# Kernel tuning notes

Measured on AMD Instinct MI355X. Metric: run time of the kernel, lower is better.

## Reference

```python
import jax, jax.numpy as jnp
import numpy as np

B, H, W, C = 16, 64, 64, 768
NH, KD = 12, 64           # num_heads, key_dim; C == NH*KD
NUM_AXES = 2              # attn_axes = [[1],[2]] -> heads split into 2 groups
SCALE = float(np.sqrt(KD))


def setup_inputs() -> dict:
    key = jax.random.key(0)
    ks = jax.random.split(key, 8)
    s = 0.02  # init scale for kernels
    return {
        "queries": jax.random.normal(ks[0], (B, H, W, C), dtype=jnp.float32),
        "values": jax.random.normal(ks[1], (B, H, W, C), dtype=jnp.float32),
        "Wq": jax.random.normal(ks[2], (C, NH, KD), dtype=jnp.float32) * s,
        "bq": jnp.zeros((NH, KD), dtype=jnp.float32),
        "Wk": jax.random.normal(ks[3], (C, NH, KD), dtype=jnp.float32) * s,
        "bk": jnp.zeros((NH, KD), dtype=jnp.float32),
        "Wv": jax.random.normal(ks[4], (C, NH, KD), dtype=jnp.float32) * s,
        "bv": jnp.zeros((NH, KD), dtype=jnp.float32),
        "Wo": jax.random.normal(ks[5], (NH, KD, C), dtype=jnp.float32) * s,
        "bo": jnp.zeros((C,), dtype=jnp.float32),
    }


def _attend_axis_h(q, k, v):
    # attention along the H axis (axis 1); q,k,v: [B,H,W,n,d]
    s = jnp.einsum('bxwnd,bhwnd->bwnhx', k, q) / SCALE  # [B,W,n,Hq,Hk]
    s = jax.nn.softmax(s, axis=-1)
    return jnp.einsum('bwnhx,bxwnd->bhwnd', s, v)


def _attend_axis_w(q, k, v):
    # attention along the W axis (axis 2); q,k,v: [B,H,W,n,d]
    s = jnp.einsum('bhynd,bhwnd->bhnwy', k, q) / SCALE  # [B,H,n,Wq,Wk]
    s = jax.nn.softmax(s, axis=-1)
    return jnp.einsum('bhnwy,bhynd->bhwnd', s, v)


def reference(queries, values, Wq, bq, Wk, bk, Wv, bv, Wo, bo):
    # QKV projections: [B,H,W,C] -> [B,H,W,NH,KD]
    q = jnp.einsum('bhwc,cnd->bhwnd', queries, Wq) + bq
    k = jnp.einsum('bhwc,cnd->bhwnd', values, Wk) + bk
    v = jnp.einsum('bhwc,cnd->bhwnd', values, Wv) + bv
    g = NH // NUM_AXES  # heads per axis group
    o0 = _attend_axis_h(q[..., :g, :], k[..., :g, :], v[..., :g, :])
    o1 = _attend_axis_w(q[..., g:, :], k[..., g:, :], v[..., g:, :])
    out = jnp.concatenate([o0, o1], axis=-2)  # [B,H,W,NH,KD]
    return jnp.einsum('bhwnd,ndc->bhwc', out, Wo) + bo
```

## Files before the change

kernel.cpp:

```cpp
#include <hip/hip_runtime.h>

typedef unsigned short u16;
typedef __bf16 bf16x8 __attribute__((ext_vector_type(8)));
typedef float f32x4 __attribute__((ext_vector_type(4)));

union BF8 {
    bf16x8 v;
    __bf16 e[8];
    u16 h[8];
};

typedef __attribute__((address_space(1))) void gvoid;
typedef __attribute__((address_space(3))) void lvoid;

__device__ __forceinline__ u16 f2bf(float f) {
    __bf16 h = (__bf16)f;
    return __builtin_bit_cast(u16, h);
}

__device__ __forceinline__ void gld_lds16(const void* g, void* l) {
    __builtin_amdgcn_global_load_lds((gvoid*)g, (lvoid*)l, 16, 0, 0);
}

__device__ __forceinline__ f32x4 mfma16(bf16x8 a, bf16x8 b, f32x4 c) {
    return __builtin_amdgcn_mfma_f32_16x16x32_bf16(a, b, c, 0, 0, 0);
}

__global__ __launch_bounds__(256) void transpose_cvt(const float* __restrict__ src,
                                                     u16* __restrict__ dst) {
    __shared__ float t[64][65];
    const int c0 = blockIdx.x * 64, r0 = blockIdx.y * 64;
    const int tid = threadIdx.x;
#pragma unroll
    for (int i = 0; i < 16; ++i) {
        int e = tid + 256 * i;
        int rr = e >> 6, cc = e & 63;
        t[rr][cc] = src[(r0 + rr) * 768 + c0 + cc];
    }
    __syncthreads();
#pragma unroll
    for (int i = 0; i < 16; ++i) {
        int e = tid + 256 * i;
        int rr = e >> 6, cc = e & 63;
        dst[(c0 + rr) * 768 + r0 + cc] = f2bf(t[cc][rr]);
    }
}

template <bool A_F32, bool OUT_F32, bool FUSE>
__global__ __launch_bounds__(256) void gemm_kernel(
    const void* __restrict__ Aptr,
    const u16* __restrict__ Bt0, const float* __restrict__ bias0, void* __restrict__ Out0,
    const u16* __restrict__ Bt1, const float* __restrict__ bias1, void* __restrict__ Out1) {
    constexpr int ASMEM = A_F32 ? 16384 : 8192;
    constexpr int J = FUSE ? 12 : 6;
    __shared__ __attribute__((aligned(16))) char smem[ASMEM + 8192];
    float* Asf = (float*)smem;
    u16* Asb = (u16*)smem;
    u16* Bs = (u16*)(smem + ASMEM);

    const int bid = blockIdx.x;
    const int xcd = bid & 7;
    const int local = bid >> 3;
    const int j = local % J;
    const int mp = xcd * 64 + local / J;

    const bool first = !FUSE || (j < 6);
    const u16* Bt = first ? Bt0 : Bt1;
    const float* bias = first ? bias0 : bias1;
    void* Out = first ? Out0 : Out1;

    const int tid = threadIdx.x;
    const int wid = tid >> 6, lane = tid & 63;
    const int quad = lane >> 4, lm = lane & 15;
    const int mbase = (wid >> 1) * 64, nbase = (wid & 1) * 64;
    const long row0 = (long)mp * 128;
    const int n0 = (FUSE ? (j % 6) : j) * 128;

    const f32x4 zero = {0.f, 0.f, 0.f, 0.f};
    f32x4 acc[4][4];
#pragma unroll
    for (int mi = 0; mi < 4; ++mi)
#pragma unroll
        for (int ni = 0; ni < 4; ++ni) acc[mi][ni] = zero;

    for (int kt = 0; kt < 24; ++kt) {
        const int k0 = kt * 32;
        if constexpr (A_F32) {
            const float* A = (const float*)Aptr;
#pragma unroll
            for (int i = 0; i < 4; ++i) {
                int chunk = tid + 256 * i;
                int m = chunk >> 3, s = chunk & 7;
                int kc = s ^ (m & 7);
                gld_lds16(A + (row0 + m) * 768 + k0 + kc * 4, Asf + chunk * 4);
            }
        } else {
            const u16* A = (const u16*)Aptr;
#pragma unroll
            for (int i = 0; i < 2; ++i) {
                int chunk = tid + 256 * i;
                int m = chunk >> 2, s = chunk & 3;
                int kc = s ^ ((m >> 1) & 3);
                gld_lds16(A + (row0 + m) * 768 + k0 + kc * 8, Asb + chunk * 8);
            }
        }
#pragma unroll
        for (int i = 0; i < 2; ++i) {
            int chunk = tid + 256 * i;
            int n = chunk >> 2, s = chunk & 3;
            int kc = s ^ ((n >> 1) & 3);
            gld_lds16(Bt + (long)(n0 + n) * 768 + k0 + kc * 8, Bs + chunk * 8);
        }
        __syncthreads();

        bf16x8 af[4], bfr[4];
#pragma unroll
        for (int mi = 0; mi < 4; ++mi) {
            int m = mbase + mi * 16 + lm;
            if constexpr (A_F32) {
                int c0 = m * 8 + ((quad * 2) ^ (m & 7));
                int c1 = m * 8 + ((quad * 2 + 1) ^ (m & 7));
                f32x4 x0 = *(const f32x4*)(Asf + c0 * 4);
                f32x4 x1 = *(const f32x4*)(Asf + c1 * 4);
                BF8 u;
#pragma unroll
                for (int jj = 0; jj < 4; ++jj) {
                    u.e[jj] = (__bf16)x0[jj];
                    u.e[4 + jj] = (__bf16)x1[jj];
                }
                af[mi] = u.v;
            } else {
                int c = m * 4 + (quad ^ ((m >> 1) & 3));
                af[mi] = *(const bf16x8*)(Asb + c * 8);
            }
        }
#pragma unroll
        for (int ni = 0; ni < 4; ++ni) {
            int n = nbase + ni * 16 + lm;
            int c = n * 4 + (quad ^ ((n >> 1) & 3));
            bfr[ni] = *(const bf16x8*)(Bs + c * 8);
        }
#pragma unroll
        for (int mi = 0; mi < 4; ++mi)
#pragma unroll
            for (int ni = 0; ni < 4; ++ni)
                acc[mi][ni] = mfma16(af[mi], bfr[ni], acc[mi][ni]);
        __syncthreads();
    }

#pragma unroll
    for (int mi = 0; mi < 4; ++mi) {
        const long row = row0 + mbase + mi * 16 + quad * 4;
#pragma unroll
        for (int ni = 0; ni < 4; ++ni) {
            const int n = n0 + nbase + ni * 16 + lm;
            const float bv = bias[n];
#pragma unroll
            for (int r = 0; r < 4; ++r) {
                float v = acc[mi][ni][r] + bv;
                if constexpr (OUT_F32)
                    ((float*)Out)[(row + r) * 768 + n] = v;
                else
                    ((u16*)Out)[(row + r) * 768 + n] = f2bf(v);
            }
        }
    }
}

__global__ __launch_bounds__(256) void attn_kernel(const u16* __restrict__ q,
                                                   const u16* __restrict__ k,
                                                   const u16* __restrict__ v,
                                                   u16* __restrict__ o) {
    __shared__ __attribute__((aligned(16))) u16 Qs[64 * 64];
    __shared__ __attribute__((aligned(16))) u16 Ks[64 * 64];
    __shared__ __attribute__((aligned(16))) u16 Vs[64 * 64];
    __shared__ __attribute__((aligned(16))) u16 Vt[64 * 72];

    const int cross = blockIdx.x;
    const int b = blockIdx.y;
    const int head = blockIdx.z;
    const bool axis0 = head < 6;
    const int tid = threadIdx.x;
    const int wid = tid >> 6, lane = tid & 63;
    const int quad = lane >> 4, lm = lane & 15;

    const long base = (long)b * 4096 + (axis0 ? cross : cross * 64);
    const int pstride = axis0 ? 64 : 1;
    const int coloff = head * 64;

#pragma unroll
    for (int i = 0; i < 2; ++i) {
        int chunk = tid + 256 * i;
        int p = chunk >> 3, s = chunk & 7;
        int c = s ^ (p & 7);
        long g = (base + (long)p * pstride) * 768 + coloff + c * 8;
        gld_lds16(q + g, Qs + chunk * 8);
        gld_lds16(k + g, Ks + chunk * 8);
        gld_lds16(v + g, Vs + chunk * 8);
    }
    __syncthreads();

#pragma unroll
    for (int i = 0; i < 2; ++i) {
        int chunk = tid + 256 * i;
        int pos = chunk & 63, cc = chunk >> 6;
        int slot = pos * 8 + (cc ^ (pos & 7));
        BF8 vv;
        vv.v = *(const bf16x8*)(Vs + slot * 8);
#pragma unroll
        for (int jj = 0; jj < 8; ++jj) Vt[(cc * 8 + jj) * 72 + pos] = vv.h[jj];
    }

    const f32x4 zero = {0.f, 0.f, 0.f, 0.f};
    f32x4 s[4];
#pragma unroll
    for (int nt = 0; nt < 4; ++nt) s[nt] = zero;

    bf16x8 qf[2];
#pragma unroll
    for (int kt = 0; kt < 2; ++kt) {
        int row = 16 * wid + lm;
        int slot = row * 8 + ((kt * 4 + quad) ^ (row & 7));
        qf[kt] = *(const bf16x8*)(Qs + slot * 8);
    }
#pragma unroll
    for (int nt = 0; nt < 4; ++nt)
#pragma unroll
        for (int kt = 0; kt < 2; ++kt) {
            int row = nt * 16 + lm;
            int slot = row * 8 + ((kt * 4 + quad) ^ (row & 7));
            bf16x8 kf = *(const bf16x8*)(Ks + slot * 8);
            s[nt] = mfma16(qf[kt], kf, s[nt]);
        }

    float invl[4];
#pragma unroll
    for (int nt = 0; nt < 4; ++nt) s[nt] = s[nt] * 0.125f;
#pragma unroll
    for (int r = 0; r < 4; ++r) {
        float m = fmaxf(fmaxf(s[0][r], s[1][r]), fmaxf(s[2][r], s[3][r]));
#pragma unroll
        for (int d = 1; d < 16; d <<= 1) m = fmaxf(m, __shfl_xor(m, d));
        float l = 0.f;
#pragma unroll
        for (int nt = 0; nt < 4; ++nt) {
            float p = exp2f((s[nt][r] - m) * 1.44269504f);
            s[nt][r] = p;
            l += p;
        }
#pragma unroll
        for (int d = 1; d < 16; d <<= 1) l += __shfl_xor(l, d);
        invl[r] = 1.f / l;
    }

#pragma unroll
    for (int nt = 0; nt < 4; ++nt)
#pragma unroll
        for (int r = 0; r < 4; ++r) {
            int h = 16 * wid + quad * 4 + r;
            int c = nt * 2 + (lm >> 3);
            Qs[(h * 8 + (c ^ (h & 7))) * 8 + (lm & 7)] = f2bf(s[nt][r]);
        }
    __syncthreads();

    f32x4 oacc[4];
#pragma unroll
    for (int nt = 0; nt < 4; ++nt) oacc[nt] = zero;
#pragma unroll
    for (int kt = 0; kt < 2; ++kt) {
        int row = 16 * wid + lm;
        int slot = row * 8 + ((kt * 4 + quad) ^ (row & 7));
        bf16x8 pf = *(const bf16x8*)(Qs + slot * 8);
#pragma unroll
        for (int nt = 0; nt < 4; ++nt) {
            bf16x8 vf = *(const bf16x8*)(Vt + (nt * 16 + lm) * 72 + kt * 32 + quad * 8);
            oacc[nt] = mfma16(pf, vf, oacc[nt]);
        }
    }

#pragma unroll
    for (int nt = 0; nt < 4; ++nt)
#pragma unroll
        for (int r = 0; r < 4; ++r) {
            int p = 16 * wid + quad * 4 + r;
            long grow = base + (long)p * pstride;
            o[grow * 768 + coloff + nt * 16 + lm] = f2bf(oacc[nt][r] * invl[r]);
        }
}

extern "C" void kernel_launch(void* const* d_in, const int* in_sizes, int n_in,
                              void* d_out, int out_size, void* d_ws, size_t ws_size,
                              hipStream_t stream) {
    const float* queries = (const float*)d_in[0];
    const float* values = (const float*)d_in[1];
    const float* Wq = (const float*)d_in[2];
    const float* bq = (const float*)d_in[3];
    const float* Wk = (const float*)d_in[4];
    const float* bk = (const float*)d_in[5];
    const float* Wv = (const float*)d_in[6];
    const float* bv = (const float*)d_in[7];
    const float* Wo = (const float*)d_in[8];
    const float* bo = (const float*)d_in[9];

    const long MAT = 65536L * 768;
    const long WMAT = 768L * 768;
    u16* qws = (u16*)d_ws;
    u16* kws = qws + MAT;
    u16* vws = kws + MAT;
    u16* aws = vws + MAT;
    u16* wtq = aws + MAT;
    u16* wtk = wtq + WMAT;
    u16* wtv = wtk + WMAT;
    u16* wto = wtv + WMAT;

    dim3 tb(256);
    dim3 tg(12, 12);
    transpose_cvt<<<tg, tb, 0, stream>>>(Wq, wtq);
    transpose_cvt<<<tg, tb, 0, stream>>>(Wk, wtk);
    transpose_cvt<<<tg, tb, 0, stream>>>(Wv, wtv);
    transpose_cvt<<<tg, tb, 0, stream>>>(Wo, wto);

    gemm_kernel<true, false, false><<<dim3(512 * 6), tb, 0, stream>>>(
        queries, wtq, bq, qws, nullptr, nullptr, nullptr);
    gemm_kernel<true, false, true><<<dim3(512 * 12), tb, 0, stream>>>(
        values, wtk, bk, kws, wtv, bv, vws);

    attn_kernel<<<dim3(64, 16, 12), tb, 0, stream>>>(qws, kws, vws, aws);

    gemm_kernel<false, true, false><<<dim3(512 * 6), tb, 0, stream>>>(
        aws, wto, bo, (float*)d_out, nullptr, nullptr, nullptr);
}
```

Measured before the change: 994.0 us.

## Double-buffer GEMM LDS tiles and pre-convert values to bf16 for fused K/V GEMM

```diff
diff --git a/kernel.cpp b/kernel.cpp
--- a/kernel.cpp
+++ b/kernel.cpp
@@ -46,17 +46,29 @@
     }
 }
 
+__global__ __launch_bounds__(256) void cvt_f32_bf16(const float* __restrict__ src,
+                                                    u16* __restrict__ dst) {
+    const long i = ((long)blockIdx.x * 256 + threadIdx.x) * 8;
+    f32x4 x0 = *(const f32x4*)(src + i);
+    f32x4 x1 = *(const f32x4*)(src + i + 4);
+    BF8 u;
+#pragma unroll
+    for (int j = 0; j < 4; ++j) {
+        u.e[j] = (__bf16)x0[j];
+        u.e[4 + j] = (__bf16)x1[j];
+    }
+    *(bf16x8*)(dst + i) = u.v;
+}
+
 template <bool A_F32, bool OUT_F32, bool FUSE>
 __global__ __launch_bounds__(256) void gemm_kernel(
     const void* __restrict__ Aptr,
     const u16* __restrict__ Bt0, const float* __restrict__ bias0, void* __restrict__ Out0,
     const u16* __restrict__ Bt1, const float* __restrict__ bias1, void* __restrict__ Out1) {
-    constexpr int ASMEM = A_F32 ? 16384 : 8192;
+    constexpr int ABUF = A_F32 ? 16384 : 8192;
+    constexpr int BUF = ABUF + 8192;
     constexpr int J = FUSE ? 12 : 6;
-    __shared__ __attribute__((aligned(16))) char smem[ASMEM + 8192];
-    float* Asf = (float*)smem;
-    u16* Asb = (u16*)smem;
-    u16* Bs = (u16*)(smem + ASMEM);
+    __shared__ __attribute__((aligned(16))) char smem[2 * BUF];
 
     const int bid = blockIdx.x;
     const int xcd = bid & 7;
@@ -76,16 +88,11 @@
     const long row0 = (long)mp * 128;
     const int n0 = (FUSE ? (j % 6) : j) * 128;
 
-    const f32x4 zero = {0.f, 0.f, 0.f, 0.f};
-    f32x4 acc[4][4];
-#pragma unroll
-    for (int mi = 0; mi < 4; ++mi)
-#pragma unroll
-        for (int ni = 0; ni < 4; ++ni) acc[mi][ni] = zero;
-
-    for (int kt = 0; kt < 24; ++kt) {
+    auto stage = [&](int buf, int kt) {
+        char* base = smem + buf * BUF;
         const int k0 = kt * 32;
         if constexpr (A_F32) {
+            float* Asf = (float*)base;
             const float* A = (const float*)Aptr;
 #pragma unroll
             for (int i = 0; i < 4; ++i) {
@@ -95,6 +102,7 @@
                 gld_lds16(A + (row0 + m) * 768 + k0 + kc * 4, Asf + chunk * 4);
             }
         } else {
+            u16* Asb = (u16*)base;
             const u16* A = (const u16*)Aptr;
 #pragma unroll
             for (int i = 0; i < 2; ++i) {
@@ -104,6 +112,7 @@
                 gld_lds16(A + (row0 + m) * 768 + k0 + kc * 8, Asb + chunk * 8);
             }
         }
+        u16* Bs = (u16*)(base + ABUF);
 #pragma unroll
         for (int i = 0; i < 2; ++i) {
             int chunk = tid + 256 * i;
@@ -111,7 +120,26 @@
             int kc = s ^ ((n >> 1) & 3);
             gld_lds16(Bt + (long)(n0 + n) * 768 + k0 + kc * 8, Bs + chunk * 8);
         }
-        __syncthreads();
+    };
+
+    const f32x4 zero = {0.f, 0.f, 0.f, 0.f};
+    f32x4 acc[4][4];
+#pragma unroll
+    for (int mi = 0; mi < 4; ++mi)
+#pragma unroll
+        for (int ni = 0; ni < 4; ++ni) acc[mi][ni] = zero;
+
+    stage(0, 0);
+    __syncthreads();
+
+    int cur = 0;
+    for (int kt = 0; kt < 24; ++kt) {
+        if (kt < 23) stage(cur ^ 1, kt + 1);
+
+        char* base = smem + cur * BUF;
+        float* Asf = (float*)base;
+        u16* Asb = (u16*)base;
+        u16* Bs = (u16*)(base + ABUF);
 
         bf16x8 af[4], bfr[4];
 #pragma unroll
@@ -145,7 +173,9 @@
 #pragma unroll
             for (int ni = 0; ni < 4; ++ni)
                 acc[mi][ni] = mfma16(af[mi], bfr[ni], acc[mi][ni]);
+
         __syncthreads();
+        cur ^= 1;
     }
 
 #pragma unroll
@@ -320,10 +350,12 @@
     transpose_cvt<<<tg, tb, 0, stream>>>(Wv, wtv);
     transpose_cvt<<<tg, tb, 0, stream>>>(Wo, wto);
 
+    cvt_f32_bf16<<<dim3(24576), tb, 0, stream>>>(values, aws);
+
     gemm_kernel<true, false, false><<<dim3(512 * 6), tb, 0, stream>>>(
         queries, wtq, bq, qws, nullptr, nullptr, nullptr);
-    gemm_kernel<true, false, true><<<dim3(512 * 12), tb, 0, stream>>>(
-        values, wtk, bk, kws, wtv, bv, vws);
+    gemm_kernel<false, false, true><<<dim3(512 * 12), tb, 0, stream>>>(
+        aws, wtk, bk, kws, wtv, bv, vws);
 
     attn_kernel<<<dim3(64, 16, 12), tb, 0, stream>>>(qws, kws, vws, aws);
 
```

Measured after the change: 979.2 us. Within noise of the previous version (-1.5%).

## Replace GEMMs with 256x256 four-stage pipelined bf16 kernel and pre-convert inputs

Applied to the files above, without the earlier changes.

```diff
diff --git a/kernel.cpp b/kernel.cpp
--- a/kernel.cpp
+++ b/kernel.cpp
@@ -46,25 +46,36 @@
     }
 }
 
-template <bool A_F32, bool OUT_F32, bool FUSE>
-__global__ __launch_bounds__(256) void gemm_kernel(
-    const void* __restrict__ Aptr,
+__global__ __launch_bounds__(256) void cvt_f32_bf16(const float* __restrict__ src,
+                                                    u16* __restrict__ dst) {
+    const long i = ((long)blockIdx.x * 256 + threadIdx.x) * 8;
+    f32x4 x0 = *(const f32x4*)(src + i);
+    f32x4 x1 = *(const f32x4*)(src + i + 4);
+    BF8 u;
+#pragma unroll
+    for (int j = 0; j < 4; ++j) {
+        u.e[j] = (__bf16)x0[j];
+        u.e[4 + j] = (__bf16)x1[j];
+    }
+    *(bf16x8*)(dst + i) = u.v;
+}
+
+template <bool OUT_F32, bool FUSE>
+__global__ __launch_bounds__(512, 2) void gemm256(
+    const u16* __restrict__ Abf,
     const u16* __restrict__ Bt0, const float* __restrict__ bias0, void* __restrict__ Out0,
     const u16* __restrict__ Bt1, const float* __restrict__ bias1, void* __restrict__ Out1) {
-    constexpr int ASMEM = A_F32 ? 16384 : 8192;
-    constexpr int J = FUSE ? 12 : 6;
-    __shared__ __attribute__((aligned(16))) char smem[ASMEM + 8192];
-    float* Asf = (float*)smem;
-    u16* Asb = (u16*)smem;
-    u16* Bs = (u16*)(smem + ASMEM);
+    constexpr int J = FUSE ? 6 : 3;
+    constexpr int NT = 24;
+    __shared__ __attribute__((aligned(16))) char smem[4 * 32768];
 
     const int bid = blockIdx.x;
     const int xcd = bid & 7;
     const int local = bid >> 3;
     const int j = local % J;
-    const int mp = xcd * 64 + local / J;
-
-    const bool first = !FUSE || (j < 6);
+    const int mp = xcd * 32 + local / J;
+
+    const bool first = !FUSE || (j < 3);
     const u16* Bt = first ? Bt0 : Bt1;
     const float* bias = first ? bias0 : bias1;
     void* Out = first ? Out0 : Out1;
@@ -72,88 +83,109 @@
     const int tid = threadIdx.x;
     const int wid = tid >> 6, lane = tid & 63;
     const int quad = lane >> 4, lm = lane & 15;
-    const int mbase = (wid >> 1) * 64, nbase = (wid & 1) * 64;
-    const long row0 = (long)mp * 128;
-    const int n0 = (FUSE ? (j % 6) : j) * 128;
+    const int wm = wid >> 2, wn = wid & 3;
+    const long row0 = (long)mp * 256;
+    const int n0 = (FUSE ? (j % 3) : j) * 256;
+
+    const int ch0 = tid, ch1 = tid + 512;
+    const int ar0 = ch0 >> 2, as0 = (ch0 & 3) ^ ((ar0 >> 1) & 3);
+    const int ar1 = ch1 >> 2, as1 = (ch1 & 3) ^ ((ar1 >> 1) & 3);
+    const u16* aSrc0 = Abf + (row0 + ar0) * 768 + as0 * 8;
+    const u16* aSrc1 = Abf + (row0 + ar1) * 768 + as1 * 8;
+    const u16* bSrc0 = Bt + (long)(n0 + ar0) * 768 + as0 * 8;
+    const u16* bSrc1 = Bt + (long)(n0 + ar1) * 768 + as1 * 8;
+
+    auto stage = [&](int t) {
+        char* base = smem + (t & 3) * 32768;
+        u16* As = (u16*)base;
+        u16* Bs = (u16*)(base + 16384);
+        const int k0 = t * 32;
+        gld_lds16(aSrc0 + k0, As + ch0 * 8);
+        gld_lds16(aSrc1 + k0, As + ch1 * 8);
+        gld_lds16(bSrc0 + k0, Bs + ch0 * 8);
+        gld_lds16(bSrc1 + k0, Bs + ch1 * 8);
+    };
+
+    bf16x8 af[8], bfr[4];
+    auto frag_read = [&](int t) {
+        const u16* As = (const u16*)(smem + (t & 3) * 32768);
+        const u16* Bs = As + 8192;
+#pragma unroll
+        for (int mi = 0; mi < 8; ++mi) {
+            int row = wm * 128 + mi * 16 + lm;
+            int c = row * 4 + (quad ^ ((row >> 1) & 3));
+            af[mi] = *(const bf16x8*)(As + c * 8);
+        }
+#pragma unroll
+        for (int ni = 0; ni < 4; ++ni) {
+            int row = wn * 64 + ni * 16 + lm;
+            int c = row * 4 + (quad ^ ((row >> 1) & 3));
+            bfr[ni] = *(const bf16x8*)(Bs + c * 8);
+        }
+    };
 
     const f32x4 zero = {0.f, 0.f, 0.f, 0.f};
-    f32x4 acc[4][4];
-#pragma unroll
-    for (int mi = 0; mi < 4; ++mi)
+    f32x4 acc[8][4];
+#pragma unroll
+    for (int mi = 0; mi < 8; ++mi)
 #pragma unroll
         for (int ni = 0; ni < 4; ++ni) acc[mi][ni] = zero;
 
-    for (int kt = 0; kt < 24; ++kt) {
-        const int k0 = kt * 32;
-        if constexpr (A_F32) {
-            const float* A = (const float*)Aptr;
-#pragma unroll
-            for (int i = 0; i < 4; ++i) {
-                int chunk = tid + 256 * i;
-                int m = chunk >> 3, s = chunk & 7;
-                int kc = s ^ (m & 7);
-                gld_lds16(A + (row0 + m) * 768 + k0 + kc * 4, Asf + chunk * 4);
-            }
-        } else {
-            const u16* A = (const u16*)Aptr;
-#pragma unroll
-            for (int i = 0; i < 2; ++i) {
-                int chunk = tid + 256 * i;
-                int m = chunk >> 2, s = chunk & 3;
-                int kc = s ^ ((m >> 1) & 3);
-                gld_lds16(A + (row0 + m) * 768 + k0 + kc * 8, Asb + chunk * 8);
-            }
-        }
-#pragma unroll
-        for (int i = 0; i < 2; ++i) {
-            int chunk = tid + 256 * i;
-            int n = chunk >> 2, s = chunk & 3;
-            int kc = s ^ ((n >> 1) & 3);
-            gld_lds16(Bt + (long)(n0 + n) * 768 + k0 + kc * 8, Bs + chunk * 8);
-        }
-        __syncthreads();
-
-        bf16x8 af[4], bfr[4];
-#pragma unroll
-        for (int mi = 0; mi < 4; ++mi) {
-            int m = mbase + mi * 16 + lm;
-            if constexpr (A_F32) {
-                int c0 = m * 8 + ((quad * 2) ^ (m & 7));
-                int c1 = m * 8 + ((quad * 2 + 1) ^ (m & 7));
-                f32x4 x0 = *(const f32x4*)(Asf + c0 * 4);
-                f32x4 x1 = *(const f32x4*)(Asf + c1 * 4);
-                BF8 u;
-#pragma unroll
-                for (int jj = 0; jj < 4; ++jj) {
-                    u.e[jj] = (__bf16)x0[jj];
-                    u.e[4 + jj] = (__bf16)x1[jj];
-                }
-                af[mi] = u.v;
-            } else {
-                int c = m * 4 + (quad ^ ((m >> 1) & 3));
-                af[mi] = *(const bf16x8*)(Asb + c * 8);
-            }
-        }
-#pragma unroll
-        for (int ni = 0; ni < 4; ++ni) {
-            int n = nbase + ni * 16 + lm;
-            int c = n * 4 + (quad ^ ((n >> 1) & 3));
-            bfr[ni] = *(const bf16x8*)(Bs + c * 8);
-        }
-#pragma unroll
-        for (int mi = 0; mi < 4; ++mi)
+    auto mfma_cluster = [&]() {
+        __builtin_amdgcn_s_setprio(1);
+#pragma unroll
+        for (int mi = 0; mi < 8; ++mi)
 #pragma unroll
             for (int ni = 0; ni < 4; ++ni)
                 acc[mi][ni] = mfma16(af[mi], bfr[ni], acc[mi][ni]);
-        __syncthreads();
-    }
-
-#pragma unroll
-    for (int mi = 0; mi < 4; ++mi) {
-        const long row = row0 + mbase + mi * 16 + quad * 4;
+        __builtin_amdgcn_s_setprio(0);
+    };
+
+    stage(0);
+    stage(1);
+    stage(2);
+    asm volatile("s_waitcnt vmcnt(8)" ::: "memory");
+    __builtin_amdgcn_sched_barrier(0);
+    __builtin_amdgcn_s_barrier();
+
+    for (int t = 0; t < 21; ++t) {
+        frag_read(t);
+        stage(t + 3);
+        __builtin_amdgcn_s_barrier();
+        asm volatile("s_waitcnt lgkmcnt(0)" ::: "memory");
+        __builtin_amdgcn_sched_barrier(0);
+        mfma_cluster();
+        asm volatile("s_waitcnt vmcnt(8)" ::: "memory");
+        __builtin_amdgcn_sched_barrier(0);
+        __builtin_amdgcn_s_barrier();
+    }
+    frag_read(21);
+    __builtin_amdgcn_s_barrier();
+    asm volatile("s_waitcnt lgkmcnt(0)" ::: "memory");
+    __builtin_amdgcn_sched_barrier(0);
+    mfma_cluster();
+    asm volatile("s_waitcnt vmcnt(4)" ::: "memory");
+    __builtin_amdgcn_sched_barrier(0);
+    __builtin_amdgcn_s_barrier();
+    frag_read(22);
+    __builtin_amdgcn_s_barrier();
+    asm volatile("s_waitcnt lgkmcnt(0)" ::: "memory");
+    __builtin_amdgcn_sched_barrier(0);
+    mfma_cluster();
+    asm volatile("s_waitcnt vmcnt(0)" ::: "memory");
+    __builtin_amdgcn_sched_barrier(0);
+    __builtin_amdgcn_s_barrier();
+    frag_read(23);
+    asm volatile("s_waitcnt lgkmcnt(0)" ::: "memory");
+    __builtin_amdgcn_sched_barrier(0);
+    mfma_cluster();
+
+#pragma unroll
+    for (int mi = 0; mi < 8; ++mi) {
+        const long row = row0 + wm * 128 + mi * 16 + quad * 4;
 #pragma unroll
         for (int ni = 0; ni < 4; ++ni) {
-            const int n = n0 + nbase + ni * 16 + lm;
+            const int n = n0 + wn * 64 + ni * 16 + lm;
             const float bv = bias[n];
 #pragma unroll
             for (int r = 0; r < 4; ++r) {
@@ -320,13 +352,17 @@
     transpose_cvt<<<tg, tb, 0, stream>>>(Wv, wtv);
     transpose_cvt<<<tg, tb, 0, stream>>>(Wo, wto);
 
-    gemm_kernel<true, false, false><<<dim3(512 * 6), tb, 0, stream>>>(
-        queries, wtq, bq, qws, nullptr, nullptr, nullptr);
-    gemm_kernel<true, false, true><<<dim3(512 * 12), tb, 0, stream>>>(
-        values, wtk, bk, kws, wtv, bv, vws);
+    dim3 tb5(512);
+    cvt_f32_bf16<<<dim3(24576), tb, 0, stream>>>(queries, aws);
+    gemm256<false, false><<<dim3(768), tb5, 0, stream>>>(
+        aws, wtq, bq, qws, nullptr, nullptr, nullptr);
+
+    cvt_f32_bf16<<<dim3(24576), tb, 0, stream>>>(values, aws);
+    gemm256<false, true><<<dim3(1536), tb5, 0, stream>>>(
+        aws, wtk, bk, kws, wtv, bv, vws);
 
     attn_kernel<<<dim3(64, 16, 12), tb, 0, stream>>>(qws, kws, vws, aws);
 
-    gemm_kernel<false, true, false><<<dim3(512 * 6), tb, 0, stream>>>(
+    gemm256<true, false><<<dim3(768), tb5, 0, stream>>>(
         aws, wto, bo, (float*)d_out, nullptr, nullptr, nullptr);
 }
```

New measurement: 965.0 us. 1.03x faster.
